# Kernel tuning notes

Measured on AMD Instinct MI355X. Metric: run time of the kernel, lower is better.

The kernel has to match this reference:

```python
import jax, jax.numpy as jnp
import numpy as np

N, D_FEAT, D, H, L = 2048, 128, 256, 8, 2
DH = D // H
E = 65536
NUM_EDGE_TYPES = 8
MAX_DIST = 10
MAX_DEGREE = 512
D_FF = 4 * D
D_OUT = 128
EPS = 1e-5


def _layernorm(x, g, b):
    mu = jnp.mean(x, axis=-1, keepdims=True)
    var = jnp.mean(jnp.square(x - mu), axis=-1, keepdims=True)
    return (x - mu) * jax.lax.rsqrt(var + EPS) * g + b


def setup_inputs() -> dict:
    key = jax.random.key(0)
    ks = jax.random.split(key, 32)
    inp = {
        "x": jax.random.normal(ks[0], (N, D_FEAT), dtype=jnp.float32),
        "edge_index": jax.random.randint(ks[1], (2, E), 0, N),
        "edge_types": jax.random.randint(ks[2], (E,), 0, NUM_EDGE_TYPES),
        "pos_encoding": jax.random.uniform(ks[3], (N, N), dtype=jnp.float32),
    }
    def xavier(k, shape):
        fan_in, fan_out = shape[0], shape[1]
        lim = float(np.sqrt(6.0 / (fan_in + fan_out)))
        return jax.random.uniform(k, shape, jnp.float32, -lim, lim)
    inp["W_emb"] = xavier(ks[4], (D_FEAT, D)); inp["b_emb"] = jnp.zeros((D,), jnp.float32)
    # stacked per-layer params, stored as [in, out] so y = x @ W + b
    inp["Wq"] = jnp.stack([xavier(jax.random.fold_in(ks[5], l), (D, D)) for l in range(L)])
    inp["Wk"] = jnp.stack([xavier(jax.random.fold_in(ks[6], l), (D, D)) for l in range(L)])
    inp["Wv"] = jnp.stack([xavier(jax.random.fold_in(ks[7], l), (D, D)) for l in range(L)])
    inp["Wo"] = jnp.stack([xavier(jax.random.fold_in(ks[8], l), (D, D)) for l in range(L)])
    for nm in ("bq", "bk", "bv", "bo"):
        inp[nm] = jnp.zeros((L, D), jnp.float32)
    inp["spd_table"] = 0.02 * jax.random.normal(ks[9], (L, MAX_DIST + 1, H), dtype=jnp.float32)
    inp["edge_table"] = 0.02 * jax.random.normal(ks[10], (L, NUM_EDGE_TYPES, H), dtype=jnp.float32)
    inp["din_emb"] = 0.02 * jax.random.normal(ks[11], (L, MAX_DEGREE + 1, D), dtype=jnp.float32)
    inp["dout_emb"] = 0.02 * jax.random.normal(ks[12], (L, MAX_DEGREE + 1, D), dtype=jnp.float32)
    inp["ln1_g"] = jnp.ones((L, D), jnp.float32); inp["ln1_b"] = jnp.zeros((L, D), jnp.float32)
    inp["ln2_g"] = jnp.ones((L, D), jnp.float32); inp["ln2_b"] = jnp.zeros((L, D), jnp.float32)
    inp["W1"] = jnp.stack([xavier(jax.random.fold_in(ks[13], l), (D, D_FF)) for l in range(L)])
    inp["b1"] = jnp.zeros((L, D_FF), jnp.float32)
    inp["W2"] = jnp.stack([xavier(jax.random.fold_in(ks[14], l), (D_FF, D)) for l in range(L)])
    inp["b2"] = jnp.zeros((L, D), jnp.float32)
    inp["W_out"] = xavier(ks[15], (D, D_OUT)); inp["b_out"] = jnp.zeros((D_OUT,), jnp.float32)
    return inp


def _forward(x, edge_index, edge_types, pos_encoding,
             W_emb, b_emb, Wq, bq, Wk, bk, Wv, bv, Wo, bo,
             spd_table, edge_table, din_emb, dout_emb,
             ln1_g, ln1_b, ln2_g, ln2_b, W1, b1, W2, b2, W_out, b_out):
    src, dst = edge_index[0], edge_index[1]
    ones = jnp.ones((E,), jnp.int32)
    deg_out = jnp.clip(jax.ops.segment_sum(ones, src, num_segments=N), 0, MAX_DEGREE)
    deg_in = jnp.clip(jax.ops.segment_sum(ones, dst, num_segments=N), 0, MAX_DEGREE)
    # SPD bucket matrix [N, N] (int), shared across layers
    spd_bucket = jnp.clip(pos_encoding[:, :N] * MAX_DIST + 0.5, 0, MAX_DIST).astype(jnp.int32)

    h = x @ W_emb + b_emb  # node embedding; dropout=0 (eval)
    scale = 1.0 / np.sqrt(DH)
    for l in range(L):
        # centrality encoding
        h = h + din_emb[l][deg_in] + dout_emb[l][deg_out]
        xn = _layernorm(h, ln1_g[l], ln1_b[l])
        q = (xn @ Wq[l] + bq[l]).reshape(N, H, DH).transpose(1, 0, 2)  # [H,N,DH]
        k = (xn @ Wk[l] + bk[l]).reshape(N, H, DH).transpose(1, 0, 2)
        v = (xn @ Wv[l] + bv[l]).reshape(N, H, DH).transpose(1, 0, 2)
        # attention bias [H, N, N]: SPD table gather + per-edge scatter-add
        bias = spd_table[l][spd_bucket].transpose(2, 0, 1)
        e_bias = edge_table[l][edge_types]  # [E, H]
        bias = bias.at[:, src, dst].add(e_bias.T)
        scores = jnp.einsum('hnd,hmd->hnm', q, k) * scale + bias
        attn = jax.nn.softmax(scores, axis=-1)
        attn_out = jnp.einsum('hnm,hmd->hnd', attn, v).transpose(1, 0, 2).reshape(N, D)
        h = h + attn_out @ Wo[l] + bo[l]
        y = _layernorm(h, ln2_g[l], ln2_b[l])
        y = jax.nn.gelu(y @ W1[l] + b1[l], approximate=False) @ W2[l] + b2[l]
        h = h + y
    return h @ W_out + b_out


def reference(x, edge_index, edge_types, pos_encoding,
              W_emb, b_emb, Wq, bq, Wk, bk, Wv, bv, Wo, bo,
              spd_table, edge_table, din_emb, dout_emb,
              ln1_g, ln1_b, ln2_g, ln2_b, W1, b1, W2, b2, W_out, b_out):
    return _forward(x, edge_index, edge_types, pos_encoding,
                    W_emb, b_emb, Wq, bq, Wk, bk, Wv, bv, Wo, bo,
                    spd_table, edge_table, din_emb, dout_emb,
                    ln1_g, ln1_b, ln2_g, ln2_b, W1, b1, W2, b2, W_out, b_out)
```

## Files before the change

kernel.cpp:

```cpp
#include <hip/hip_runtime.h>
#include <math.h>

#define N_NODES 2048
#define D_MODEL 256
#define D_FEAT 128
#define NHEAD 8
#define DH 32
#define NLAYER 2
#define NEDGE 65536
#define D_FF 1024
#define D_OUT 128
#define MAXDEG 512
#define JSPLIT 4

typedef __attribute__((ext_vector_type(8))) short short8;
typedef __attribute__((ext_vector_type(4))) float f32x4;
typedef __attribute__((ext_vector_type(4))) unsigned short u16x4;

__device__ __forceinline__ unsigned short f2bf(float f) {
    unsigned u = __float_as_uint(f);
    unsigned r = (u + 0x7FFFu + ((u >> 16) & 1u)) >> 16;
    return (unsigned short)r;
}

template <int CTRL>
__device__ __forceinline__ float dpp_ror(float x) {
    return __int_as_float(__builtin_amdgcn_update_dpp(0, __float_as_int(x), CTRL, 0xf, 0xf, false));
}

__device__ __forceinline__ void wt_tile(const float* __restrict__ W, unsigned short* __restrict__ Wt,
                                        int K, int Nc, int n0, int k0, int tid,
                                        unsigned short (*tile)[33]) {
    int r = tid >> 3, cg = (tid & 7) * 4;
    float4 w4 = *(const float4*)&W[(size_t)(k0 + r) * Nc + n0 + cg];
    tile[r][cg + 0] = f2bf(w4.x); tile[r][cg + 1] = f2bf(w4.y);
    tile[r][cg + 2] = f2bf(w4.z); tile[r][cg + 3] = f2bf(w4.w);
    __syncthreads();
    int c = tid >> 3, rg = (tid & 7) * 4;
    u16x4 o;
    #pragma unroll
    for (int j = 0; j < 4; j++) o[j] = tile[rg + j][c];
    *(u16x4*)&Wt[(size_t)(n0 + c) * K + k0 + rg] = o;
}

__global__ void mega_prep_kernel(const float* __restrict__ pos, unsigned char* __restrict__ bucket,
                                 unsigned* __restrict__ hist, int* __restrict__ deg_out,
                                 int* __restrict__ deg_in, unsigned* __restrict__ gcursor,
                                 const float* __restrict__ Wq, const float* __restrict__ Wk,
                                 const float* __restrict__ Wv, const float* __restrict__ Wo,
                                 const float* __restrict__ W1, const float* __restrict__ W2,
                                 const float* __restrict__ W_emb, const float* __restrict__ W_out,
                                 const float* __restrict__ bq, const float* __restrict__ bk,
                                 const float* __restrict__ bv,
                                 unsigned short* __restrict__ qkvt, unsigned short* __restrict__ wot,
                                 unsigned short* __restrict__ w1t, unsigned short* __restrict__ w2t,
                                 unsigned short* __restrict__ wembt, unsigned short* __restrict__ woutt,
                                 float* __restrict__ bqkv) {
    __shared__ unsigned short tile[32][33];
    int b = blockIdx.x, tid = threadIdx.x;
    if (b < 4096) {
        int i = b * 256 + tid;
        float4 p = *(const float4*)&pos[(size_t)i * 4];
        unsigned b0 = (unsigned)fminf(fmaxf(p.x * 10.f + 0.5f, 0.f), 10.f);
        unsigned b1 = (unsigned)fminf(fmaxf(p.y * 10.f + 0.5f, 0.f), 10.f);
        unsigned b2 = (unsigned)fminf(fmaxf(p.z * 10.f + 0.5f, 0.f), 10.f);
        unsigned b3 = (unsigned)fminf(fmaxf(p.w * 10.f + 0.5f, 0.f), 10.f);
        ((unsigned*)bucket)[i] = b0 | (b1 << 8) | (b2 << 16) | (b3 << 24);
        if (b < 64) {
            #pragma unroll
            for (int k = 0; k < 4; k++) hist[b * 1024 + k * 256 + tid] = 0;
        } else if (b == 64) {
            #pragma unroll
            for (int k = 0; k < 8; k++) deg_out[k * 256 + tid] = 0;
            #pragma unroll
            for (int k = 0; k < 8; k++) deg_in[k * 256 + tid] = 0;
            if (tid == 0) *gcursor = 0;
        }
        return;
    }
    int bb = b - 4096;
    if (bb < 512) {
        int z = bb >> 6, t = bb & 63;
        int l = z >> 2, which = z & 3;
        const float* W = (which == 0 ? Wq : which == 1 ? Wk : which == 2 ? Wv : Wo) + (size_t)l * 65536;
        unsigned short* dst = (which < 3) ? qkvt + (size_t)l * 196608 + which * 65536
                                          : wot + (size_t)l * 65536;
        wt_tile(W, dst, 256, 256, (t & 7) * 32, (t >> 3) * 32, tid, tile);
    } else if (bb < 1024) {
        int b2 = bb - 512, l = b2 >> 8, t = b2 & 255;
        wt_tile(W1 + (size_t)l * D_MODEL * D_FF, w1t + (size_t)l * D_MODEL * D_FF,
                D_MODEL, D_FF, (t & 31) * 32, (t >> 5) * 32, tid, tile);
    } else if (bb < 1536) {
        int b3 = bb - 1024, l = b3 >> 8, t = b3 & 255;
        wt_tile(W2 + (size_t)l * D_FF * D_MODEL, w2t + (size_t)l * D_FF * D_MODEL,
                D_FF, D_MODEL, (t & 7) * 32, (t >> 3) * 32, tid, tile);
    } else if (bb < 1568) {
        int b4 = bb - 1536;
        wt_tile(W_emb, wembt, D_FEAT, D_MODEL, (b4 & 7) * 32, (b4 >> 3) * 32, tid, tile);
    } else if (bb < 1600) {
        int b5 = bb - 1568;
        wt_tile(W_out, woutt, D_MODEL, D_OUT, (b5 & 3) * 32, (b5 >> 2) * 32, tid, tile);
    } else {
        int i = (bb - 1600) * 256 + tid;
        if (i < NLAYER * 768) {
            int l = i / 768, j = i % 768;
            const float* src = j < 256 ? bq : j < 512 ? bk : bv;
            bqkv[i] = src[l * 256 + (j & 255)];
        }
    }
}

__global__ void degree_hist_kernel(const int* __restrict__ ei,
                                   int* __restrict__ deg_out, int* __restrict__ deg_in,
                                   unsigned* __restrict__ hist) {
    int e = blockIdx.x * 256 + threadIdx.x;
    if (e < NEDGE) {
        int src = ei[e], dst = ei[NEDGE + e];
        atomicAdd(&deg_out[src], 1);
        atomicAdd(&deg_in[dst], 1);
        atomicAdd(&hist[(src >> 6) * 2048 + dst], 1);
    }
}

__global__ void edge_alloc_kernel(const unsigned* __restrict__ hist,
                                  unsigned* __restrict__ offsets, unsigned* __restrict__ cursor,
                                  unsigned* __restrict__ gend, unsigned* __restrict__ gcursor) {
    int g = blockIdx.x;
    int t = threadIdx.x;
    unsigned v = hist[g * 64 + t];
    unsigned inc = v;
    #pragma unroll
    for (int off = 1; off < 64; off <<= 1) {
        unsigned u = __shfl_up(inc, off);
        if (t >= off) inc += u;
    }
    unsigned total = __shfl(inc, 63);
    unsigned base = 0;
    if (t == 63) base = atomicAdd(gcursor, total);
    base = __shfl(base, 63);
    unsigned o = base + inc - v;
    offsets[g * 64 + t] = o;
    cursor[g * 64 + t] = o;
    if (t == 63) gend[g] = base + total;
}

__global__ void edge_scatter_kernel(const int* __restrict__ ei, const int* __restrict__ etypes,
                                    unsigned* __restrict__ cursor, unsigned* __restrict__ packed) {
    int e = blockIdx.x * 256 + threadIdx.x;
    if (e < NEDGE) {
        int src = ei[e], dst = ei[NEDGE + e];
        int key = (src >> 6) * 2048 + dst;
        unsigned pos = atomicAdd(&cursor[key], 1);
        packed[pos] = (unsigned)dst | ((unsigned)(src & 63) << 11) | ((unsigned)etypes[e] << 17);
    }
}

__global__ void centrality_ln_kernel(float* __restrict__ h,
                                     const float* __restrict__ din_l,
                                     const float* __restrict__ dout_l,
                                     const int* __restrict__ deg_in,
                                     const int* __restrict__ deg_out,
                                     const float* __restrict__ g,
                                     const float* __restrict__ b,
                                     unsigned short* __restrict__ y) {
    int row = blockIdx.x;
    int tid = threadIdx.x;
    int di = min(max(deg_in[row], 0), MAXDEG);
    int dn = min(max(deg_out[row], 0), MAXDEG);
    float v = h[row * D_MODEL + tid] + din_l[di * D_MODEL + tid] + dout_l[dn * D_MODEL + tid];
    h[row * D_MODEL + tid] = v;
    __shared__ float red[256];
    red[tid] = v; __syncthreads();
    for (int s = 128; s > 0; s >>= 1) { if (tid < s) red[tid] += red[tid + s]; __syncthreads(); }
    float mu = red[0] * (1.0f / D_MODEL);
    __syncthreads();
    float d = v - mu;
    red[tid] = d * d; __syncthreads();
    for (int s = 128; s > 0; s >>= 1) { if (tid < s) red[tid] += red[tid + s]; __syncthreads(); }
    float rstd = rsqrtf(red[0] * (1.0f / D_MODEL) + 1e-5f);
    y[row * D_MODEL + tid] = f2bf(d * rstd * g[tid] + b[tid]);
}

__global__ void layernorm_kernel(const float* __restrict__ x,
                                 const float* __restrict__ g,
                                 const float* __restrict__ b,
                                 unsigned short* __restrict__ y) {
    int row = blockIdx.x;
    int tid = threadIdx.x;
    float v = x[row * D_MODEL + tid];
    __shared__ float red[256];
    red[tid] = v; __syncthreads();
    for (int s = 128; s > 0; s >>= 1) { if (tid < s) red[tid] += red[tid + s]; __syncthreads(); }
    float mu = red[0] * (1.0f / D_MODEL);
    __syncthreads();
    float d = v - mu;
    red[tid] = d * d; __syncthreads();
    for (int s = 128; s > 0; s >>= 1) { if (tid < s) red[tid] += red[tid + s]; __syncthreads(); }
    float rstd = rsqrtf(red[0] * (1.0f / D_MODEL) + 1e-5f);
    y[row * D_MODEL + tid] = f2bf(d * rstd * g[tid] + b[tid]);
}

template <int ACT, bool RESID, bool OUTBF16, bool AFP32>
__global__ void gemm_mfma_kernel(const void* __restrict__ Av,
                                 const unsigned short* __restrict__ Wt,
                                 const float* __restrict__ bias,
                                 float* __restrict__ C, unsigned short* __restrict__ Cb,
                                 int Nc, int K) {
    __shared__ __align__(16) unsigned short As[32][72];
    __shared__ __align__(16) unsigned short Bs[64][72];
    const unsigned short* A16 = (const unsigned short*)Av;
    const float* A32 = (const float*)Av;
    int tid = threadIdx.x;
    int m0 = blockIdx.y * 32, n0 = blockIdx.x * 64;
    int w = tid >> 6, lane = tid & 63;
    int rg = (w & 1) * 16, cg = (w >> 1) * 32;
    int m = lane & 15, quad = lane >> 4;
    f32x4 acc[2] = {{0.f, 0.f, 0.f, 0.f}, {0.f, 0.f, 0.f, 0.f}};
    int ar = tid >> 3, ac = (tid & 7) * 8;
    uint4 ra; float4 fa0, fa1; uint4 rb0, rb1;
    if (AFP32) {
        fa0 = *(const float4*)&A32[(size_t)(m0 + ar) * K + ac];
        fa1 = *(const float4*)&A32[(size_t)(m0 + ar) * K + ac + 4];
    } else {
        ra = *(const uint4*)&A16[(size_t)(m0 + ar) * K + ac];
    }
    rb0 = *(const uint4*)&Wt[(size_t)(n0 + ar) * K + ac];
    rb1 = *(const uint4*)&Wt[(size_t)(n0 + 32 + ar) * K + ac];
    for (int k0 = 0; k0 < K; k0 += 64) {
        if (AFP32) {
            u16x4 t0 = {f2bf(fa0.x), f2bf(fa0.y), f2bf(fa0.z), f2bf(fa0.w)};
            u16x4 t1 = {f2bf(fa1.x), f2bf(fa1.y), f2bf(fa1.z), f2bf(fa1.w)};
            *(u16x4*)&As[ar][ac] = t0;
            *(u16x4*)&As[ar][ac + 4] = t1;
        } else {
            *(uint4*)&As[ar][ac] = ra;
        }
        *(uint4*)&Bs[ar][ac] = rb0;
        *(uint4*)&Bs[ar + 32][ac] = rb1;
        __syncthreads();
        int kn = k0 + 64;
        if (kn < K) {
            if (AFP32) {
                fa0 = *(const float4*)&A32[(size_t)(m0 + ar) * K + kn + ac];
                fa1 = *(const float4*)&A32[(size_t)(m0 + ar) * K + kn + ac + 4];
            } else {
                ra = *(const uint4*)&A16[(size_t)(m0 + ar) * K + kn + ac];
            }
            rb0 = *(const uint4*)&Wt[(size_t)(n0 + ar) * K + kn + ac];
            rb1 = *(const uint4*)&Wt[(size_t)(n0 + 32 + ar) * K + kn + ac];
        }
        #pragma unroll
        for (int ks = 0; ks < 2; ks++) {
            short8 a = *(const short8*)&As[rg + m][ks * 32 + quad * 8];
            #pragma unroll
            for (int t = 0; t < 2; t++) {
                short8 b = *(const short8*)&Bs[cg + t * 16 + m][ks * 32 + quad * 8];
                acc[t] = __builtin_amdgcn_mfma_f32_16x16x32_bf16(a, b, acc[t], 0, 0, 0);
            }
        }
        __syncthreads();
    }
    #pragma unroll
    for (int t = 0; t < 2; t++) {
        #pragma unroll
        for (int reg = 0; reg < 4; reg++) {
            int row = m0 + rg + quad * 4 + reg;
            int col = n0 + cg + t * 16 + m;
            float val = acc[t][reg] + bias[col];
            if (ACT == 1) val = val * 0.5f * (1.0f + erff(val * 0.7071067811865476f));
            size_t idx = (size_t)row * Nc + col;
            if (RESID) val += C[idx];
            if (OUTBF16) Cb[idx] = f2bf(val);
            else C[idx] = val;
        }
    }
}

__global__ void gemm_oproj_kernel(const float* __restrict__ part_O,
                                  const float* __restrict__ l_part,
                                  const unsigned short* __restrict__ Wt,
                                  const float* __restrict__ bias,
                                  float* __restrict__ C) {
    __shared__ __align__(16) unsigned short As[32][72];
    __shared__ __align__(16) unsigned short Bs[64][72];
    int tid = threadIdx.x;
    int m0 = blockIdx.y * 32, n0 = blockIdx.x * 64;
    int w = tid >> 6, lane = tid & 63;
    int rg = (w & 1) * 16, cg = (w >> 1) * 32;
    int m = lane & 15, quad = lane >> 4;
    f32x4 acc[2] = {{0.f, 0.f, 0.f, 0.f}, {0.f, 0.f, 0.f, 0.f}};
    int ar = tid >> 3, ac = (tid & 7) * 8;
    int row = m0 + ar;
    for (int k0 = 0; k0 < D_MODEL; k0 += 64) {
        int col = k0 + ac;
        int hh = col >> 5;
        float L = 0.f;
        float o[8] = {0.f, 0.f, 0.f, 0.f, 0.f, 0.f, 0.f, 0.f};
        #pragma unroll
        for (int js = 0; js < JSPLIT; js++) {
            L += l_part[((size_t)js * NHEAD + hh) * N_NODES + row];
            const float* pp = &part_O[((size_t)js * N_NODES + row) * D_MODEL + col];
            float4 p0 = *(const float4*)pp;
            float4 p1 = *(const float4*)(pp + 4);
            o[0] += p0.x; o[1] += p0.y; o[2] += p0.z; o[3] += p0.w;
            o[4] += p1.x; o[5] += p1.y; o[6] += p1.z; o[7] += p1.w;
        }
        float inv = 1.0f / L;
        u16x4 t0, t1;
        #pragma unroll
        for (int j = 0; j < 4; j++) { t0[j] = f2bf(o[j] * inv); t1[j] = f2bf(o[j + 4] * inv); }
        *(u16x4*)&As[ar][ac] = t0;
        *(u16x4*)&As[ar][ac + 4] = t1;
        *(uint4*)&Bs[ar][ac] = *(const uint4*)&Wt[(size_t)(n0 + ar) * D_MODEL + k0 + ac];
        *(uint4*)&Bs[ar + 32][ac] = *(const uint4*)&Wt[(size_t)(n0 + 32 + ar) * D_MODEL + k0 + ac];
        __syncthreads();
        #pragma unroll
        for (int ks = 0; ks < 2; ks++) {
            short8 a = *(const short8*)&As[rg + m][ks * 32 + quad * 8];
            #pragma unroll
            for (int t = 0; t < 2; t++) {
                short8 b = *(const short8*)&Bs[cg + t * 16 + m][ks * 32 + quad * 8];
                acc[t] = __builtin_amdgcn_mfma_f32_16x16x32_bf16(a, b, acc[t], 0, 0, 0);
            }
        }
        __syncthreads();
    }
    #pragma unroll
    for (int t = 0; t < 2; t++) {
        #pragma unroll
        for (int reg = 0; reg < 4; reg++) {
            int orow = m0 + rg + quad * 4 + reg;
            int ocol = n0 + cg + t * 16 + m;
            size_t idx = (size_t)orow * D_MODEL + ocol;
            C[idx] += acc[t][reg] + bias[ocol];
        }
    }
}

template <int ACT, bool VOUT>
__global__ void gemm64_kernel(const unsigned short* __restrict__ A,
                              const unsigned short* __restrict__ Wt,
                              const float* __restrict__ bias,
                              unsigned short* __restrict__ Cb,
                              unsigned short* __restrict__ vbt,
                              int Nc, int K) {
    __shared__ __align__(16) unsigned short As[64][72];
    __shared__ __align__(16) unsigned short Bs[64][72];
    int tid = threadIdx.x;
    int m0 = blockIdx.y * 64, n0 = blockIdx.x * 64;
    int w = tid >> 6, lane = tid & 63;
    int wr = (w & 1) * 32, wc = (w >> 1) * 32;
    int m = lane & 15, quad = lane >> 4;
    f32x4 acc[2][2] = {{{0.f,0.f,0.f,0.f},{0.f,0.f,0.f,0.f}},{{0.f,0.f,0.f,0.f},{0.f,0.f,0.f,0.f}}};
    int sr = tid >> 2, sg = (tid & 3) * 16;
    uint4 a0 = *(const uint4*)&A[(size_t)(m0 + sr) * K + sg];
    uint4 a1 = *(const uint4*)&A[(size_t)(m0 + sr) * K + sg + 8];
    uint4 b0 = *(const uint4*)&Wt[(size_t)(n0 + sr) * K + sg];
    uint4 b1 = *(const uint4*)&Wt[(size_t)(n0 + sr) * K + sg + 8];
    for (int k0 = 0; k0 < K; k0 += 64) {
        *(uint4*)&As[sr][sg] = a0;
        *(uint4*)&As[sr][sg + 8] = a1;
        *(uint4*)&Bs[sr][sg] = b0;
        *(uint4*)&Bs[sr][sg + 8] = b1;
        __syncthreads();
        int kn = k0 + 64;
        if (kn < K) {
            a0 = *(const uint4*)&A[(size_t)(m0 + sr) * K + kn + sg];
            a1 = *(const uint4*)&A[(size_t)(m0 + sr) * K + kn + sg + 8];
            b0 = *(const uint4*)&Wt[(size_t)(n0 + sr) * K + kn + sg];
            b1 = *(const uint4*)&Wt[(size_t)(n0 + sr) * K + kn + sg + 8];
        }
        #pragma unroll
        for (int kh = 0; kh < 2; kh++) {
            short8 x0 = *(const short8*)&As[wr + m][kh * 32 + quad * 8];
            short8 x1 = *(const short8*)&As[wr + 16 + m][kh * 32 + quad * 8];
            short8 y0 = *(const short8*)&Bs[wc + m][kh * 32 + quad * 8];
            short8 y1 = *(const short8*)&Bs[wc + 16 + m][kh * 32 + quad * 8];
            acc[0][0] = __builtin_amdgcn_mfma_f32_16x16x32_bf16(x0, y0, acc[0][0], 0, 0, 0);
            acc[0][1] = __builtin_amdgcn_mfma_f32_16x16x32_bf16(x0, y1, acc[0][1], 0, 0, 0);
            acc[1][0] = __builtin_amdgcn_mfma_f32_16x16x32_bf16(x1, y0, acc[1][0], 0, 0, 0);
            acc[1][1] = __builtin_amdgcn_mfma_f32_16x16x32_bf16(x1, y1, acc[1][1], 0, 0, 0);
        }
        __syncthreads();
    }
    if (VOUT && n0 >= 512) {
        #pragma unroll
        for (int mt = 0; mt < 2; mt++) {
            #pragma unroll
            for (int nt = 0; nt < 2; nt++) {
                int cl = wc + nt * 16 + m;
                float bcol = bias[n0 + cl];
                #pragma unroll
                for (int reg = 0; reg < 4; reg++)
                    As[cl][wr + mt * 16 + quad * 4 + reg] = f2bf(acc[mt][nt][reg] + bcol);
            }
        }
        __syncthreads();
        int rr = tid >> 2, cc = (tid & 3) * 16;
        uint4 o0 = *(const uint4*)&As[rr][cc];
        uint4 o1 = *(const uint4*)&As[rr][cc + 8];
        *(uint4*)&vbt[(size_t)(n0 - 512 + rr) * N_NODES + m0 + cc] = o0;
        *(uint4*)&vbt[(size_t)(n0 - 512 + rr) * N_NODES + m0 + cc + 8] = o1;
        return;
    }
    #pragma unroll
    for (int mt = 0; mt < 2; mt++) {
        #pragma unroll
        for (int nt = 0; nt < 2; nt++) {
            #pragma unroll
            for (int reg = 0; reg < 4; reg++) {
                int row = m0 + wr + mt * 16 + quad * 4 + reg;
                int col = n0 + wc + nt * 16 + m;
                float val = acc[mt][nt][reg] + bias[col];
                if (ACT == 1) val = val * 0.5f * (1.0f + erff(val * 0.7071067811865476f));
                Cb[(size_t)row * Nc + col] = f2bf(val);
            }
        }
    }
}

__global__ __launch_bounds__(256)
void flash_attn_kernel(const unsigned short* __restrict__ qkvb,
                       const unsigned short* __restrict__ vbt,
                       const unsigned char* __restrict__ bucket,
                       const float* __restrict__ spd_l,
                       const float* __restrict__ et_l,
                       const unsigned* __restrict__ offsets,
                       const unsigned* __restrict__ gend,
                       const unsigned* __restrict__ packed,
                       float* __restrict__ part_O,
                       float* __restrict__ l_part) {
    __shared__ __align__(16) unsigned short ks[64][40];
    __shared__ __align__(16) unsigned short vs[32][72];
    __shared__ __align__(16) float ov[64][68];
    __shared__ float et[8];

    int tid = threadIdx.x;
    int rb = blockIdx.x;
    int i0 = rb * 64;
    int hh = blockIdx.y;
    int js = blockIdx.z;
    int lane = tid & 63;
    if (tid < 8) et[tid] = et_l[tid * NHEAD + hh];
    float spd_reg = spd_l[(lane < 11 ? lane : 10) * NHEAD + hh];

    int w = tid >> 6;
    int m = lane & 15, quad = lane >> 4;
    int r0 = w * 16;
    short8 aq = *(const short8*)&qkvb[(size_t)(i0 + r0 + m) * 768 + hh * DH + quad * 8];
    float l_st[4] = {0.f, 0.f, 0.f, 0.f};
    f32x4 oacc[2] = {{0.f, 0.f, 0.f, 0.f}, {0.f, 0.f, 0.f, 0.f}};
    const float scale = 0.17677669529663687f;
    const int NT = N_NODES / JSPLIT / 64;

    int krow = tid >> 2, kcol = (tid & 3) * 8;
    int vrow = tid >> 3, vcol = (tid & 7) * 8;
    int brow = tid >> 2, bcol = (tid & 3) * 16;

    int jbase = js * (N_NODES / JSPLIT);
    uint4 kpre = *(const uint4*)&qkvb[(size_t)(jbase + krow) * 768 + 256 + hh * DH + kcol];
    uint4 vpre = *(const uint4*)&vbt[(size_t)(hh * DH + vrow) * N_NODES + jbase + vcol];
    uint4 bpre = *(const uint4*)&bucket[(size_t)(i0 + brow) * N_NODES + jbase + bcol];

    for (int jt = 0; jt < NT; jt++) {
        int j0 = jbase + jt * 64;
        *(uint4*)&ks[krow][kcol] = kpre;
        *(uint4*)&vs[vrow][vcol] = vpre;
        {
            const unsigned char* bb = (const unsigned char*)&bpre;
            float fb[16];
            #pragma unroll
            for (int i = 0; i < 16; i++)
                fb[i] = __int_as_float(
                    __builtin_amdgcn_ds_bpermute(((int)bb[i]) << 2, __float_as_int(spd_reg)));
            #pragma unroll
            for (int g = 0; g < 4; g++) {
                f32x4 st = {fb[g * 4], fb[g * 4 + 1], fb[g * 4 + 2], fb[g * 4 + 3]};
                *(f32x4*)&ov[brow][bcol + g * 4] = st;
            }
        }
        __syncthreads();
        if (jt + 1 < NT) {
            int jn = j0 + 64;
            kpre = *(const uint4*)&qkvb[(size_t)(jn + krow) * 768 + 256 + hh * DH + kcol];
            vpre = *(const uint4*)&vbt[(size_t)(hh * DH + vrow) * N_NODES + jn + vcol];
            bpre = *(const uint4*)&bucket[(size_t)(i0 + brow) * N_NODES + jn + bcol];
        }
        {
            unsigned key0 = (unsigned)rb * 2048 + j0;
            unsigned start = offsets[key0], end = gend[key0 >> 6];
            for (unsigned i = start + tid; i < end; i += 256) {
                unsigned p = packed[i];
                atomicAdd(&ov[(p >> 11) & 63][(p & 2047) - j0], et[(p >> 17) & 7]);
            }
        }
        __syncthreads();
        float sv[4][4];
        #pragma unroll
        for (int t = 0; t < 4; t++) {
            short8 bk8 = *(const short8*)&ks[t * 16 + m][quad * 8];
            f32x4 z = {0.f, 0.f, 0.f, 0.f};
            f32x4 sacc = __builtin_amdgcn_mfma_f32_16x16x32_bf16(aq, bk8, z, 0, 0, 0);
            #pragma unroll
            for (int r = 0; r < 4; r++)
                sv[t][r] = __expf(sacc[r] * scale + ov[r0 + quad * 4 + r][t * 16 + m]);
        }
        #pragma unroll
        for (int r = 0; r < 4; r++) {
            float ps = sv[0][r] + sv[1][r] + sv[2][r] + sv[3][r];
            ps += dpp_ror<0x121>(ps);
            ps += dpp_ror<0x122>(ps);
            ps += dpp_ror<0x124>(ps);
            ps += dpp_ror<0x128>(ps);
            l_st[r] += ps;
        }
        #pragma unroll
        for (int t = 0; t < 4; t++)
            #pragma unroll
            for (int r = 0; r < 4; r++)
                ov[r0 + quad * 4 + r][t * 16 + m] = sv[t][r];
        __builtin_amdgcn_s_waitcnt(0xC07F);
        #pragma unroll
        for (int kh = 0; kh < 2; kh++) {
            f32x4 p0 = *(const f32x4*)&ov[r0 + m][kh * 32 + quad * 8];
            f32x4 p1 = *(const f32x4*)&ov[r0 + m][kh * 32 + quad * 8 + 4];
            short8 pa;
            pa[0] = (short)f2bf(p0[0]); pa[1] = (short)f2bf(p0[1]);
            pa[2] = (short)f2bf(p0[2]); pa[3] = (short)f2bf(p0[3]);
            pa[4] = (short)f2bf(p1[0]); pa[5] = (short)f2bf(p1[1]);
            pa[6] = (short)f2bf(p1[2]); pa[7] = (short)f2bf(p1[3]);
            #pragma unroll
            for (int t = 0; t < 2; t++) {
                short8 vb = *(const short8*)&vs[t * 16 + m][kh * 32 + quad * 8];
                oacc[t] = __builtin_amdgcn_mfma_f32_16x16x32_bf16(pa, vb, oacc[t], 0, 0, 0);
            }
        }
        __syncthreads();
    }
    #pragma unroll
    for (int t = 0; t < 2; t++)
        #pragma unroll
        for (int r = 0; r < 4; r++)
            part_O[((size_t)js * N_NODES + i0 + r0 + quad * 4 + r) * D_MODEL + hh * DH + t * 16 + m] =
                oacc[t][r];
    if (m == 0) {
        #pragma unroll
        for (int r = 0; r < 4; r++) {
            int row = i0 + r0 + quad * 4 + r;
            l_part[((size_t)js * NHEAD + hh) * N_NODES + row] = l_st[r];
        }
    }
}

#define WS_ALLOC(type, name, count) \
    type* name = (type*)base; base += (((size_t)(count) * sizeof(type)) + 255) & ~(size_t)255;

extern "C" void kernel_launch(void* const* d_in, const int* in_sizes, int n_in,
                              void* d_out, int out_size, void* d_ws, size_t ws_size,
                              hipStream_t stream) {
    const float* x          = (const float*)d_in[0];
    const int*   edge_index = (const int*)d_in[1];
    const int*   edge_types = (const int*)d_in[2];
    const float* pos        = (const float*)d_in[3];
    const float* W_emb      = (const float*)d_in[4];
    const float* b_emb      = (const float*)d_in[5];
    const float* Wq         = (const float*)d_in[6];
    const float* Wk         = (const float*)d_in[7];
    const float* Wv         = (const float*)d_in[8];
    const float* Wo         = (const float*)d_in[9];
    const float* bq         = (const float*)d_in[10];
    const float* bk         = (const float*)d_in[11];
    const float* bv         = (const float*)d_in[12];
    const float* bo         = (const float*)d_in[13];
    const float* spd_table  = (const float*)d_in[14];
    const float* edge_table = (const float*)d_in[15];
    const float* din_emb    = (const float*)d_in[16];
    const float* dout_emb   = (const float*)d_in[17];
    const float* ln1_g      = (const float*)d_in[18];
    const float* ln1_b      = (const float*)d_in[19];
    const float* ln2_g      = (const float*)d_in[20];
    const float* ln2_b      = (const float*)d_in[21];
    const float* W1         = (const float*)d_in[22];
    const float* b1         = (const float*)d_in[23];
    const float* W2         = (const float*)d_in[24];
    const float* b2         = (const float*)d_in[25];
    const float* W_out      = (const float*)d_in[26];
    const float* b_out      = (const float*)d_in[27];
    float* out = (float*)d_out;

    char* base = (char*)d_ws;
    WS_ALLOC(int, deg_out, N_NODES)
    WS_ALLOC(int, deg_in, N_NODES)
    WS_ALLOC(float, h, N_NODES * D_MODEL)
    WS_ALLOC(unsigned short, xb, N_NODES * D_MODEL)
    WS_ALLOC(unsigned short, qkvb, N_NODES * 768)
    WS_ALLOC(unsigned short, vbt, D_MODEL * N_NODES)
    WS_ALLOC(unsigned short, ffnb, N_NODES * D_FF)
    WS_ALLOC(unsigned char, bucket, (size_t)N_NODES * N_NODES)
    WS_ALLOC(unsigned short, qkvt, NLAYER * 768 * D_MODEL)
    WS_ALLOC(unsigned short, wot, NLAYER * D_MODEL * D_MODEL)
    WS_ALLOC(unsigned short, w1t, NLAYER * D_MODEL * D_FF)
    WS_ALLOC(unsigned short, w2t, NLAYER * D_FF * D_MODEL)
    WS_ALLOC(unsigned short, wembt, D_FEAT * D_MODEL)
    WS_ALLOC(unsigned short, woutt, D_MODEL * D_OUT)
    WS_ALLOC(float, bqkv, NLAYER * 768)
    WS_ALLOC(unsigned, hist, 65536)
    WS_ALLOC(unsigned, offsets, 65536)
    WS_ALLOC(unsigned, cursor, 65536)
    WS_ALLOC(unsigned, gend, 1024)
    WS_ALLOC(unsigned, gcursor, 1)
    WS_ALLOC(unsigned, packed, NEDGE)
    WS_ALLOC(float, part_O, (size_t)JSPLIT * N_NODES * D_MODEL)
    WS_ALLOC(float, l_part, (size_t)JSPLIT * NHEAD * N_NODES)

    mega_prep_kernel<<<5702, 256, 0, stream>>>(pos, bucket, hist, deg_out, deg_in, gcursor,
                                               Wq, Wk, Wv, Wo, W1, W2, W_emb, W_out,
                                               bq, bk, bv, qkvt, wot, w1t, w2t, wembt, woutt, bqkv);
    degree_hist_kernel<<<NEDGE / 256, 256, 0, stream>>>(edge_index, deg_out, deg_in, hist);
    edge_alloc_kernel<<<1024, 64, 0, stream>>>(hist, offsets, cursor, gend, gcursor);
    edge_scatter_kernel<<<NEDGE / 256, 256, 0, stream>>>(edge_index, edge_types, cursor, packed);

    gemm_mfma_kernel<0, false, false, true><<<dim3(D_MODEL / 64, N_NODES / 32), 256, 0, stream>>>(
        x, wembt, b_emb, h, nullptr, D_MODEL, D_FEAT);

    for (int l = 0; l < NLAYER; l++) {
        centrality_ln_kernel<<<N_NODES, 256, 0, stream>>>(
            h, din_emb + (size_t)l * (MAXDEG + 1) * D_MODEL,
            dout_emb + (size_t)l * (MAXDEG + 1) * D_MODEL, deg_in, deg_out,
            ln1_g + l * D_MODEL, ln1_b + l * D_MODEL, xb);

        gemm64_kernel<0, true><<<dim3(768 / 64, N_NODES / 64), 256, 0, stream>>>(
            xb, qkvt + (size_t)l * 768 * D_MODEL, bqkv + l * 768, qkvb, vbt, 768, D_MODEL);

        flash_attn_kernel<<<dim3(N_NODES / 64, NHEAD, JSPLIT), 256, 0, stream>>>(
            qkvb, vbt, bucket, spd_table + (size_t)l * 11 * NHEAD,
            edge_table + (size_t)l * 8 * NHEAD, offsets, gend, packed, part_O, l_part);

        gemm_oproj_kernel<<<dim3(D_MODEL / 64, N_NODES / 32), 256, 0, stream>>>(
            part_O, l_part, wot + (size_t)l * D_MODEL * D_MODEL, bo + l * D_MODEL, h);

        layernorm_kernel<<<N_NODES, 256, 0, stream>>>(h, ln2_g + l * D_MODEL, ln2_b + l * D_MODEL, xb);

        gemm64_kernel<1, false><<<dim3(D_FF / 64, N_NODES / 64), 256, 0, stream>>>(
            xb, w1t + (size_t)l * D_MODEL * D_FF, b1 + l * D_FF, ffnb, nullptr, D_FF, D_MODEL);

        gemm_mfma_kernel<0, true, false, false><<<dim3(D_MODEL / 64, N_NODES / 32), 256, 0, stream>>>(
            ffnb, w2t + (size_t)l * D_FF * D_MODEL, b2 + l * D_MODEL, h, nullptr, D_MODEL, D_FF);
    }

    gemm_mfma_kernel<0, false, false, true><<<dim3(D_OUT / 64, N_NODES / 32), 256, 0, stream>>>(
        h, woutt, b_out, out, nullptr, D_OUT, D_MODEL);
}
```

Before: 302.5 us.

## Fuse centrality add and layernorms into QKV and FFN1 GEMM prologues

```diff
diff --git a/kernel.cpp b/kernel.cpp
--- a/kernel.cpp
+++ b/kernel.cpp
@@ -155,51 +155,6 @@
     }
 }
 
-__global__ void centrality_ln_kernel(float* __restrict__ h,
-                                     const float* __restrict__ din_l,
-                                     const float* __restrict__ dout_l,
-                                     const int* __restrict__ deg_in,
-                                     const int* __restrict__ deg_out,
-                                     const float* __restrict__ g,
-                                     const float* __restrict__ b,
-                                     unsigned short* __restrict__ y) {
-    int row = blockIdx.x;
-    int tid = threadIdx.x;
-    int di = min(max(deg_in[row], 0), MAXDEG);
-    int dn = min(max(deg_out[row], 0), MAXDEG);
-    float v = h[row * D_MODEL + tid] + din_l[di * D_MODEL + tid] + dout_l[dn * D_MODEL + tid];
-    h[row * D_MODEL + tid] = v;
-    __shared__ float red[256];
-    red[tid] = v; __syncthreads();
-    for (int s = 128; s > 0; s >>= 1) { if (tid < s) red[tid] += red[tid + s]; __syncthreads(); }
-    float mu = red[0] * (1.0f / D_MODEL);
-    __syncthreads();
-    float d = v - mu;
-    red[tid] = d * d; __syncthreads();
-    for (int s = 128; s > 0; s >>= 1) { if (tid < s) red[tid] += red[tid + s]; __syncthreads(); }
-    float rstd = rsqrtf(red[0] * (1.0f / D_MODEL) + 1e-5f);
-    y[row * D_MODEL + tid] = f2bf(d * rstd * g[tid] + b[tid]);
-}
-
-__global__ void layernorm_kernel(const float* __restrict__ x,
-                                 const float* __restrict__ g,
-                                 const float* __restrict__ b,
-                                 unsigned short* __restrict__ y) {
-    int row = blockIdx.x;
-    int tid = threadIdx.x;
-    float v = x[row * D_MODEL + tid];
-    __shared__ float red[256];
-    red[tid] = v; __syncthreads();
-    for (int s = 128; s > 0; s >>= 1) { if (tid < s) red[tid] += red[tid + s]; __syncthreads(); }
-    float mu = red[0] * (1.0f / D_MODEL);
-    __syncthreads();
-    float d = v - mu;
-    red[tid] = d * d; __syncthreads();
-    for (int s = 128; s > 0; s >>= 1) { if (tid < s) red[tid] += red[tid + s]; __syncthreads(); }
-    float rstd = rsqrtf(red[0] * (1.0f / D_MODEL) + 1e-5f);
-    y[row * D_MODEL + tid] = f2bf(d * rstd * g[tid] + b[tid]);
-}
-
 template <int ACT, bool RESID, bool OUTBF16, bool AFP32>
 __global__ void gemm_mfma_kernel(const void* __restrict__ Av,
                                  const unsigned short* __restrict__ Wt,
@@ -280,6 +235,10 @@
                                   const float* __restrict__ l_part,
                                   const unsigned short* __restrict__ Wt,
                                   const float* __restrict__ bias,
+                                  const float* __restrict__ din_l,
+                                  const float* __restrict__ dout_l,
+                                  const int* __restrict__ deg_in,
+                                  const int* __restrict__ deg_out,
                                   float* __restrict__ C) {
     __shared__ __align__(16) unsigned short As[32][72];
     __shared__ __align__(16) unsigned short Bs[64][72];
@@ -325,25 +284,41 @@
         }
         __syncthreads();
     }
+    int dio[4], dno[4];
+    #pragma unroll
+    for (int reg = 0; reg < 4; reg++) {
+        int orow = m0 + rg + quad * 4 + reg;
+        dio[reg] = min(max(deg_in[orow], 0), MAXDEG);
+        dno[reg] = min(max(deg_out[orow], 0), MAXDEG);
+    }
     #pragma unroll
     for (int t = 0; t < 2; t++) {
         #pragma unroll
         for (int reg = 0; reg < 4; reg++) {
             int orow = m0 + rg + quad * 4 + reg;
             int ocol = n0 + cg + t * 16 + m;
+            float cent = din_l[(size_t)dio[reg] * D_MODEL + ocol] +
+                         dout_l[(size_t)dno[reg] * D_MODEL + ocol];
             size_t idx = (size_t)orow * D_MODEL + ocol;
-            C[idx] += acc[t][reg] + bias[ocol];
-        }
-    }
-}
-
-template <int ACT, bool VOUT>
-__global__ void gemm64_kernel(const unsigned short* __restrict__ A,
-                              const unsigned short* __restrict__ Wt,
-                              const float* __restrict__ bias,
-                              unsigned short* __restrict__ Cb,
-                              unsigned short* __restrict__ vbt,
-                              int Nc, int K) {
+            C[idx] += cent + acc[t][reg] + bias[ocol];
+        }
+    }
+}
+
+template <int ACT, bool VOUT, bool CENT>
+__global__ void gemm64_ln_kernel(const float* __restrict__ H,
+                                 const float* __restrict__ din_l,
+                                 const float* __restrict__ dout_l,
+                                 const int* __restrict__ deg_in,
+                                 const int* __restrict__ deg_out,
+                                 const float* __restrict__ lng,
+                                 const float* __restrict__ lnb,
+                                 const unsigned short* __restrict__ Wt,
+                                 const float* __restrict__ bias,
+                                 unsigned short* __restrict__ Cb,
+                                 unsigned short* __restrict__ vbt,
+                                 int Nc) {
+    const int K = D_MODEL;
     __shared__ __align__(16) unsigned short As[64][72];
     __shared__ __align__(16) unsigned short Bs[64][72];
     int tid = threadIdx.x;
@@ -353,22 +328,77 @@
     int m = lane & 15, quad = lane >> 4;
     f32x4 acc[2][2] = {{{0.f,0.f,0.f,0.f},{0.f,0.f,0.f,0.f}},{{0.f,0.f,0.f,0.f},{0.f,0.f,0.f,0.f}}};
     int sr = tid >> 2, sg = (tid & 3) * 16;
-    uint4 a0 = *(const uint4*)&A[(size_t)(m0 + sr) * K + sg];
-    uint4 a1 = *(const uint4*)&A[(size_t)(m0 + sr) * K + sg + 8];
-    uint4 b0 = *(const uint4*)&Wt[(size_t)(n0 + sr) * K + sg];
-    uint4 b1 = *(const uint4*)&Wt[(size_t)(n0 + sr) * K + sg + 8];
+    int arow = m0 + sr;
+    int di = 0, dn = 0;
+    if (CENT) {
+        di = min(max(deg_in[arow], 0), MAXDEG);
+        dn = min(max(deg_out[arow], 0), MAXDEG);
+    }
+    int q = tid & 3;
+    float sum = 0.f, ss = 0.f;
+    #pragma unroll
+    for (int c = 0; c < 64; c += 4) {
+        int col = q * 64 + c;
+        float4 hv = *(const float4*)&H[(size_t)arow * K + col];
+        if (CENT) {
+            float4 d1 = *(const float4*)&din_l[(size_t)di * K + col];
+            float4 d2 = *(const float4*)&dout_l[(size_t)dn * K + col];
+            hv.x += d1.x + d2.x; hv.y += d1.y + d2.y;
+            hv.z += d1.z + d2.z; hv.w += d1.w + d2.w;
+        }
+        sum += hv.x + hv.y + hv.z + hv.w;
+        ss += hv.x * hv.x + hv.y * hv.y + hv.z * hv.z + hv.w * hv.w;
+    }
+    sum += __shfl_xor(sum, 1); ss += __shfl_xor(ss, 1);
+    sum += __shfl_xor(sum, 2); ss += __shfl_xor(ss, 2);
+    float mu = sum * (1.0f / K);
+    float rstd = rsqrtf(ss * (1.0f / K) - mu * mu + 1e-5f);
+    float4 ha0, ha1, ha2, ha3;
+    float4 da0 = {0,0,0,0}, da1 = {0,0,0,0}, da2 = {0,0,0,0}, da3 = {0,0,0,0};
+    float4 ea0 = {0,0,0,0}, ea1 = {0,0,0,0}, ea2 = {0,0,0,0}, ea3 = {0,0,0,0};
+    uint4 rb0, rb1;
+    auto loadA = [&](int kk) {
+        const float* hp = &H[(size_t)arow * K + kk + sg];
+        ha0 = *(const float4*)hp;       ha1 = *(const float4*)(hp + 4);
+        ha2 = *(const float4*)(hp + 8); ha3 = *(const float4*)(hp + 12);
+        if (CENT) {
+            const float* d1 = &din_l[(size_t)di * K + kk + sg];
+            const float* d2 = &dout_l[(size_t)dn * K + kk + sg];
+            da0 = *(const float4*)d1;       da1 = *(const float4*)(d1 + 4);
+            da2 = *(const float4*)(d1 + 8); da3 = *(const float4*)(d1 + 12);
+            ea0 = *(const float4*)d2;       ea1 = *(const float4*)(d2 + 4);
+            ea2 = *(const float4*)(d2 + 8); ea3 = *(const float4*)(d2 + 12);
+        }
+    };
+    loadA(0);
+    rb0 = *(const uint4*)&Wt[(size_t)(n0 + sr) * K + sg];
+    rb1 = *(const uint4*)&Wt[(size_t)(n0 + sr) * K + sg + 8];
     for (int k0 = 0; k0 < K; k0 += 64) {
-        *(uint4*)&As[sr][sg] = a0;
-        *(uint4*)&As[sr][sg + 8] = a1;
-        *(uint4*)&Bs[sr][sg] = b0;
-        *(uint4*)&Bs[sr][sg + 8] = b1;
+        int cb = k0 + sg;
+        #define STAGE1(HV, DV, EV, off) { \
+            float4 gg = *(const float4*)&lng[cb + off]; \
+            float4 bv = *(const float4*)&lnb[cb + off]; \
+            float vx = HV.x, vy = HV.y, vz = HV.z, vw = HV.w; \
+            if (CENT) { vx += DV.x + EV.x; vy += DV.y + EV.y; vz += DV.z + EV.z; vw += DV.w + EV.w; } \
+            u16x4 o; \
+            o[0] = f2bf((vx - mu) * rstd * gg.x + bv.x); \
+            o[1] = f2bf((vy - mu) * rstd * gg.y + bv.y); \
+            o[2] = f2bf((vz - mu) * rstd * gg.z + bv.z); \
+            o[3] = f2bf((vw - mu) * rstd * gg.w + bv.w); \
+            *(u16x4*)&As[sr][sg + off] = o; }
+        STAGE1(ha0, da0, ea0, 0)
+        STAGE1(ha1, da1, ea1, 4)
+        STAGE1(ha2, da2, ea2, 8)
+        STAGE1(ha3, da3, ea3, 12)
+        #undef STAGE1
+        *(uint4*)&Bs[sr][sg] = rb0;
+        *(uint4*)&Bs[sr][sg + 8] = rb1;
         __syncthreads();
         int kn = k0 + 64;
         if (kn < K) {
-            a0 = *(const uint4*)&A[(size_t)(m0 + sr) * K + kn + sg];
-            a1 = *(const uint4*)&A[(size_t)(m0 + sr) * K + kn + sg + 8];
-            b0 = *(const uint4*)&Wt[(size_t)(n0 + sr) * K + kn + sg];
-            b1 = *(const uint4*)&Wt[(size_t)(n0 + sr) * K + kn + sg + 8];
+            loadA(kn);
+            rb0 = *(const uint4*)&Wt[(size_t)(n0 + sr) * K + kn + sg];
+            rb1 = *(const uint4*)&Wt[(size_t)(n0 + sr) * K + kn + sg + 8];
         }
         #pragma unroll
         for (int kh = 0; kh < 2; kh++) {
@@ -624,25 +654,24 @@
         x, wembt, b_emb, h, nullptr, D_MODEL, D_FEAT);
 
     for (int l = 0; l < NLAYER; l++) {
-        centrality_ln_kernel<<<N_NODES, 256, 0, stream>>>(
-            h, din_emb + (size_t)l * (MAXDEG + 1) * D_MODEL,
-            dout_emb + (size_t)l * (MAXDEG + 1) * D_MODEL, deg_in, deg_out,
-            ln1_g + l * D_MODEL, ln1_b + l * D_MODEL, xb);
-
-        gemm64_kernel<0, true><<<dim3(768 / 64, N_NODES / 64), 256, 0, stream>>>(
-            xb, qkvt + (size_t)l * 768 * D_MODEL, bqkv + l * 768, qkvb, vbt, 768, D_MODEL);
+        const float* din_l = din_emb + (size_t)l * (MAXDEG + 1) * D_MODEL;
+        const float* dout_l = dout_emb + (size_t)l * (MAXDEG + 1) * D_MODEL;
+
+        gemm64_ln_kernel<0, true, true><<<dim3(768 / 64, N_NODES / 64), 256, 0, stream>>>(
+            h, din_l, dout_l, deg_in, deg_out, ln1_g + l * D_MODEL, ln1_b + l * D_MODEL,
+            qkvt + (size_t)l * 768 * D_MODEL, bqkv + l * 768, qkvb, vbt, 768);
 
         flash_attn_kernel<<<dim3(N_NODES / 64, NHEAD, JSPLIT), 256, 0, stream>>>(
             qkvb, vbt, bucket, spd_table + (size_t)l * 11 * NHEAD,
             edge_table + (size_t)l * 8 * NHEAD, offsets, gend, packed, part_O, l_part);
 
         gemm_oproj_kernel<<<dim3(D_MODEL / 64, N_NODES / 32), 256, 0, stream>>>(
-            part_O, l_part, wot + (size_t)l * D_MODEL * D_MODEL, bo + l * D_MODEL, h);
-
-        layernorm_kernel<<<N_NODES, 256, 0, stream>>>(h, ln2_g + l * D_MODEL, ln2_b + l * D_MODEL, xb);
-
-        gemm64_kernel<1, false><<<dim3(D_FF / 64, N_NODES / 64), 256, 0, stream>>>(
-            xb, w1t + (size_t)l * D_MODEL * D_FF, b1 + l * D_FF, ffnb, nullptr, D_FF, D_MODEL);
+            part_O, l_part, wot + (size_t)l * D_MODEL * D_MODEL, bo + l * D_MODEL,
+            din_l, dout_l, deg_in, deg_out, h);
+
+        gemm64_ln_kernel<1, false, false><<<dim3(D_FF / 64, N_NODES / 64), 256, 0, stream>>>(
+            h, nullptr, nullptr, nullptr, nullptr, ln2_g + l * D_MODEL, ln2_b + l * D_MODEL,
+            w1t + (size_t)l * D_MODEL * D_FF, b1 + l * D_FF, ffnb, nullptr, D_FF);
 
         gemm_mfma_kernel<0, true, false, false><<<dim3(D_MODEL / 64, N_NODES / 32), 256, 0, stream>>>(
             ffnb, w2t + (size_t)l * D_FF * D_MODEL, b2 + l * D_MODEL, h, nullptr, D_MODEL, D_FF);
```

Measured after the change: 355.0 us. +17.3%, slower.
